# Optimization experiments

Hardware: AMD Instinct MI355X
Metric: run time of the kernel (lower is better)

Reference implementation:

```python
import jax, jax.numpy as jnp
import numpy as np

N_NODES = 50000
EPS_BN = 1e-5


def _glorot(key, shape):
    fan_in, fan_out = shape[0], shape[1]
    lim = jnp.sqrt(6.0 / (fan_in + fan_out))
    return jax.random.uniform(key, shape, jnp.float32, -lim, lim)


def setup_inputs() -> dict:
    key = jax.random.key(0)
    ks = jax.random.split(key, 12)
    x = jax.random.normal(ks[0], (N_NODES, 128), jnp.float32)
    y = jax.random.normal(ks[1], (256, 1), jnp.float32)
    edge_index = jax.random.randint(ks[2], (2, 800000), 0, N_NODES, jnp.int64)
    return {
        "x": x,
        "y": y,
        "edge_index": edge_index,
        # GCNConv weights (in_dim, out_dim) + bias
        "W1": _glorot(ks[3], (128, 128)), "b1": jnp.zeros((128,), jnp.float32),
        "W2": _glorot(ks[4], (128, 128)), "b2": jnp.zeros((128,), jnp.float32),
        "W3": _glorot(ks[5], (128, 64)),  "b3": jnp.zeros((64,), jnp.float32),
        # target MLP: BatchNorm1d(1) -> Linear(1,128) -> ReLU -> Dropout -> Linear(128,64)
        "bn_gamma": jnp.ones((1,), jnp.float32), "bn_beta": jnp.zeros((1,), jnp.float32),
        "Wm1": _glorot(ks[6], (1, 128)),  "bm1": jnp.zeros((128,), jnp.float32),
        "Wm2": _glorot(ks[7], (128, 64)), "bm2": jnp.zeros((64,), jnp.float32),
    }


def gcn_conv(h, W, b, src, dst, deg_isqrt, n):
    # PyG GCNConv: x' = D^-1/2 (A+I) D^-1/2 (x W) + b, self-loops included in src/dst
    h = h @ W  # [n, out]
    norm = (deg_isqrt[src] * deg_isqrt[dst])[:, None]  # [E, 1]
    msg = h[src] * norm  # gather + scale, [E, out]
    out = jax.ops.segment_sum(msg, dst, num_segments=n)  # scatter-add
    return out + b


def reference(x, y, edge_index, W1, b1, W2, b2, W3, b3, bn_gamma, bn_beta, Wm1, bm1, Wm2, bm2):
    n = x.shape[0]
    loops = jnp.arange(n, dtype=edge_index.dtype)
    src = jnp.concatenate([edge_index[0], loops])
    dst = jnp.concatenate([edge_index[1], loops])
    deg = jax.ops.segment_sum(jnp.ones_like(dst, dtype=x.dtype), dst, num_segments=n)
    deg_isqrt = jnp.where(deg > 0, jax.lax.rsqrt(deg), 0.0)

    h = jax.nn.relu(gcn_conv(x, W1, b1, src, dst, deg_isqrt, n))
    h = jax.nn.relu(gcn_conv(h, W2, b2, src, dst, deg_isqrt, n))
    h = gcn_conv(h, W3, b3, src, dst, deg_isqrt, n)
    # transform_feat: normalize per-node embeddings (global_mean_pool result is discarded in source)
    x_emb = h / jnp.clip(jnp.linalg.norm(h, axis=1, keepdims=True), 1e-12)

    # target branch: BatchNorm1d (training-mode batch stats), Linear, ReLU, Dropout(eval=id), Linear
    mu = jnp.mean(y, axis=0, keepdims=True)
    var = jnp.var(y, axis=0, keepdims=True)
    yb = (y - mu) * jax.lax.rsqrt(var + EPS_BN) * bn_gamma + bn_beta
    t = jax.nn.relu(yb @ Wm1 + bm1)
    t = t @ Wm2 + bm2
    y_emb = t / jnp.clip(jnp.linalg.norm(t, axis=1, keepdims=True), 1e-12)
    return (x_emb, y_emb)
```

## Files before the change

kernel.cpp:

```cpp
#include <hip/hip_runtime.h>
#include <hip/hip_bf16.h>

typedef __attribute__((ext_vector_type(8))) short short8;
typedef __attribute__((ext_vector_type(4))) float f32x4;

__device__ __forceinline__ ushort f2bf(float f) {
    union { float f; uint u; } v; v.f = f;
    uint u = v.u;
    return (ushort)((u + 0x7fffu + ((u >> 16) & 1u)) >> 16);
}
__device__ __forceinline__ float bf_lo(uint u) { return __uint_as_float(u << 16); }
__device__ __forceinline__ float bf_hi(uint u) { return __uint_as_float(u & 0xffff0000u); }
__device__ __forceinline__ float lane_bcast_f(float v, int j) {
    return __uint_as_float(__builtin_amdgcn_readlane(__float_as_uint(v), j));
}

template <int COLS, bool F32IN>
__device__ __forceinline__ void gemm_body(const void* __restrict__ Xin,
                                          const ushort* __restrict__ Wt,
                                          ushort* __restrict__ Y, int n,
                                          int bid, char* smem) {
    constexpr int LDW = 136;
    ushort* sX = (ushort*)smem;
    ushort* sW = sX + 64 * LDW;
    const int tid = threadIdx.x;
    const int row0 = bid * 64;

    if (F32IN) {
        const float* Xf = (const float*)Xin;
#pragma unroll
        for (int i = 0; i < 8; ++i) {
            int idx = i * 256 + tid;
            int r = idx >> 5, kc = idx & 31;
            int gr = min(row0 + r, n - 1);
            float4 v = *(const float4*)&Xf[(size_t)gr * 128 + kc * 4];
            ushort4 o;
            o.x = f2bf(v.x); o.y = f2bf(v.y); o.z = f2bf(v.z); o.w = f2bf(v.w);
            *(ushort4*)&sX[r * LDW + kc * 4] = o;
        }
    } else {
        const ushort* Xb = (const ushort*)Xin;
#pragma unroll
        for (int i = 0; i < 4; ++i) {
            int idx = i * 256 + tid;
            int r = idx >> 4, kc = idx & 15;
            int gr = min(row0 + r, n - 1);
            uint4 v = *(const uint4*)&Xb[(size_t)gr * 128 + kc * 8];
            *(uint4*)&sX[r * LDW + kc * 8] = v;
        }
    }
#pragma unroll
    for (int c = tid; c < COLS * 16; c += 256) {
        int r = c >> 4, kc = c & 15;
        uint4 v = *(const uint4*)&Wt[(size_t)r * 128 + kc * 8];
        *(uint4*)&sW[r * LDW + kc * 8] = v;
    }
    __syncthreads();

    constexpr int NT = (COLS == 128) ? 2 : 1;
    constexpr int WN = COLS / 4;
    const int w = tid >> 6;
    const int lane = tid & 63;
    const int lm = lane & 15;
    const int kq = lane >> 4;

    f32x4 acc[4][NT];
#pragma unroll
    for (int mt = 0; mt < 4; ++mt)
#pragma unroll
        for (int ntn = 0; ntn < NT; ++ntn) acc[mt][ntn] = (f32x4){0.f, 0.f, 0.f, 0.f};

#pragma unroll
    for (int ks = 0; ks < 4; ++ks) {
        const int k0 = ks * 32 + kq * 8;
        short8 bfr[NT];
#pragma unroll
        for (int ntn = 0; ntn < NT; ++ntn)
            bfr[ntn] = *(const short8*)&sW[(w * WN + ntn * 16 + lm) * LDW + k0];
#pragma unroll
        for (int mt = 0; mt < 4; ++mt) {
            short8 afr = *(const short8*)&sX[(mt * 16 + lm) * LDW + k0];
#pragma unroll
            for (int ntn = 0; ntn < NT; ++ntn)
                acc[mt][ntn] = __builtin_amdgcn_mfma_f32_16x16x32_bf16(afr, bfr[ntn], acc[mt][ntn], 0, 0, 0);
        }
    }

#pragma unroll
    for (int mt = 0; mt < 4; ++mt) {
        int r_base = row0 + mt * 16 + kq * 4;
#pragma unroll
        for (int ntn = 0; ntn < NT; ++ntn) {
            int col = w * WN + ntn * 16 + lm;
#pragma unroll
            for (int rr = 0; rr < 4; ++rr) {
                int r = r_base + rr;
                if (r < n) Y[(size_t)r * COLS + col] = f2bf(acc[mt][ntn][rr]);
            }
        }
    }
}

#define PCHUNK 4096

__global__ __launch_bounds__(256) void k_partition(const int* __restrict__ src,
                                                   const int* __restrict__ dst, int E,
                                                   int nbuck, int cap, int pblocks,
                                                   int* __restrict__ gcur,
                                                   uint* __restrict__ part,
                                                   const float* __restrict__ W1,
                                                   const float* __restrict__ W2,
                                                   const float* __restrict__ W3,
                                                   ushort* __restrict__ wt1,
                                                   ushort* __restrict__ wt2,
                                                   ushort* __restrict__ wt3) {
    __shared__ int hist[256];
    __shared__ int base[256];
    __shared__ int cnt2[256];
    const int tid = threadIdx.x;

    if ((int)blockIdx.x >= pblocks) {
        int i = (blockIdx.x - pblocks) * 256 + tid;
        if (i < 16384) {
            int k = i >> 7, nn = i & 127;
            wt1[nn * 128 + k] = f2bf(W1[i]);
        } else if (i < 32768) {
            int j = i - 16384;
            int k = j >> 7, nn = j & 127;
            wt2[nn * 128 + k] = f2bf(W2[j]);
        } else if (i < 40960) {
            int j = i - 32768;
            int k = j >> 6, nn = j & 63;
            wt3[nn * 128 + k] = f2bf(W3[j]);
        }
        return;
    }

    const int s0 = blockIdx.x * PCHUNK;
    const int send = min(s0 + PCHUNK, E);
    hist[tid] = 0;
    cnt2[tid] = 0;
    __syncthreads();
    for (int i = s0 + tid; i < send; i += 256) {
        int d = dst[i];
        atomicAdd(&hist[d >> 8], 1);
    }
    __syncthreads();
    if (tid < nbuck && hist[tid] > 0) base[tid] = atomicAdd(&gcur[tid], hist[tid]);
    __syncthreads();
    for (int i = s0 + tid; i < send; i += 256) {
        int d = dst[i];
        int s = src[i];
        int k = d >> 8;
        int r = base[k] + atomicAdd(&cnt2[k], 1);
        if (r < cap) part[(size_t)k * cap + r] = ((uint)d << 16) | (uint)s;
    }
}

__global__ __launch_bounds__(256) void k_sort_gemm1(const uint* __restrict__ part,
                                                    const int* __restrict__ gcur,
                                                    int nbuck, int cap, int n,
                                                    int* __restrict__ rowptr,
                                                    float* __restrict__ dis,
                                                    int* __restrict__ csr,
                                                    const float* __restrict__ x,
                                                    const ushort* __restrict__ wt1,
                                                    ushort* __restrict__ bufA) {
    __shared__ char smem[(64 + 128) * 136 * 2];
    const int tid = threadIdx.x;

    if ((int)blockIdx.x >= nbuck) {
        gemm_body<128, true>(x, wt1, bufA, n, blockIdx.x - nbuck, smem);
        return;
    }

    int* hist  = (int*)smem;
    int* pfx   = hist + 256;
    int* sscan = pfx + 256;
    const int b = blockIdx.x;

    int gv = (tid < nbuck) ? min(gcur[tid], cap) : 0;
    sscan[tid] = gv;
    __syncthreads();
    for (int off = 1; off < 256; off <<= 1) {
        int t = (tid >= off) ? sscan[tid - off] : 0;
        __syncthreads();
        sscan[tid] += t;
        __syncthreads();
    }
    const int outbase = (b == 0) ? 0 : sscan[b - 1];
    const int sz = min(gcur[b], cap);
    const uint* seg = part + (size_t)b * cap;

    hist[tid] = 0;
    __syncthreads();
    for (int i = tid; i < sz; i += 256) atomicAdd(&hist[(seg[i] >> 16) & 255], 1);
    __syncthreads();

    int cnt_t = hist[tid];
    pfx[tid] = cnt_t;
    __syncthreads();
    for (int off = 1; off < 256; off <<= 1) {
        int t = (tid >= off) ? pfx[tid - off] : 0;
        __syncthreads();
        pfx[tid] += t;
        __syncthreads();
    }
    int excl = pfx[tid] - cnt_t;

    int node = b * 256 + tid;
    if (node < n) {
        rowptr[node] = outbase + excl;
        dis[node] = rsqrtf((float)(cnt_t + 1));
        if (node == n - 1) rowptr[n] = outbase + excl + cnt_t;
    }
    __syncthreads();
    pfx[tid] = excl;
    hist[tid] = 0;
    __syncthreads();
    for (int i = tid; i < sz; i += 256) {
        uint p = seg[i];
        int j = (p >> 16) & 255;
        int r = atomicAdd(&hist[j], 1);
        csr[outbase + pfx[j] + r] = (int)(p & 0xffffu);
    }
}

template <int COLS>
__global__ __launch_bounds__(512) void agg_gemm(const ushort* __restrict__ H,
                                                const float* __restrict__ dis,
                                                const int* __restrict__ rowptr,
                                                const int* __restrict__ csr,
                                                const float* __restrict__ bias,
                                                const ushort* __restrict__ Wt,
                                                ushort* __restrict__ Y, int n) {
    __shared__ ushort sX[64 * 136];
    const int tid = threadIdx.x;
    const int wv = tid >> 6;
    const int lane = tid & 63;
    const int row0 = blockIdx.x * 64;
    const uint* Hu = (const uint*)H;
    const float2 bv = ((const float2*)bias)[lane];

#pragma unroll 1
    for (int i = 0; i < 8; ++i) {
        const int lr = wv * 8 + i;
        const int v = min(row0 + lr, n - 1);
        const float dv = dis[v];
        const int e0 = rowptr[v];
        const int e1 = rowptr[v + 1];
        uint h0 = Hu[(size_t)v * 64 + lane];
        float ax = dv * bf_lo(h0), ay = dv * bf_hi(h0);

        int e = e0;
        while (e < e1) {
            const int c = min(e1 - e, 64);
            int sidx = 0; float sw = 0.0f;
            if (lane < c) { sidx = csr[e + lane]; sw = dis[sidx]; }
            int j = 0;
            for (; j + 16 <= c; j += 16) {
                uint hv[16]; float wgt[16];
#pragma unroll
                for (int u = 0; u < 16; ++u) {
                    int s = __builtin_amdgcn_readlane(sidx, j + u);
                    wgt[u] = lane_bcast_f(sw, j + u);
                    hv[u] = Hu[(size_t)s * 64 + lane];
                }
#pragma unroll
                for (int u = 0; u < 16; ++u) { ax += wgt[u] * bf_lo(hv[u]); ay += wgt[u] * bf_hi(hv[u]); }
            }
            for (; j + 4 <= c; j += 4) {
                uint hv[4]; float wgt[4];
#pragma unroll
                for (int u = 0; u < 4; ++u) {
                    int s = __builtin_amdgcn_readlane(sidx, j + u);
                    wgt[u] = lane_bcast_f(sw, j + u);
                    hv[u] = Hu[(size_t)s * 64 + lane];
                }
#pragma unroll
                for (int u = 0; u < 4; ++u) { ax += wgt[u] * bf_lo(hv[u]); ay += wgt[u] * bf_hi(hv[u]); }
            }
            for (; j < c; ++j) {
                int s = __builtin_amdgcn_readlane(sidx, j);
                float wg = lane_bcast_f(sw, j);
                uint hh = Hu[(size_t)s * 64 + lane];
                ax += wg * bf_lo(hh); ay += wg * bf_hi(hh);
            }
            e += c;
        }

        float rx = fmaxf(dv * ax + bv.x, 0.f);
        float ry = fmaxf(dv * ay + bv.y, 0.f);
        ((uint*)sX)[lr * 68 + lane] = (uint)f2bf(rx) | ((uint)f2bf(ry) << 16);
    }
    __syncthreads();

    constexpr int NT = COLS / 64;
    constexpr int WN = COLS / 4;
    const int wr = wv >> 2;
    const int wc = wv & 3;
    const int lm = lane & 15;
    const int kq = lane >> 4;

    f32x4 acc[2][NT];
#pragma unroll
    for (int mt = 0; mt < 2; ++mt)
#pragma unroll
        for (int ntn = 0; ntn < NT; ++ntn) acc[mt][ntn] = (f32x4){0.f, 0.f, 0.f, 0.f};

#pragma unroll
    for (int ks = 0; ks < 4; ++ks) {
        const int k0 = ks * 32 + kq * 8;
        short8 bfr[NT];
#pragma unroll
        for (int ntn = 0; ntn < NT; ++ntn)
            bfr[ntn] = *(const short8*)&Wt[(size_t)(wc * WN + ntn * 16 + lm) * 128 + k0];
#pragma unroll
        for (int mt = 0; mt < 2; ++mt) {
            short8 afr = *(const short8*)&sX[((wr * 2 + mt) * 16 + lm) * 136 + k0];
#pragma unroll
            for (int ntn = 0; ntn < NT; ++ntn)
                acc[mt][ntn] = __builtin_amdgcn_mfma_f32_16x16x32_bf16(afr, bfr[ntn], acc[mt][ntn], 0, 0, 0);
        }
    }

#pragma unroll
    for (int mt = 0; mt < 2; ++mt) {
        int r_base = row0 + (wr * 2 + mt) * 16 + kq * 4;
#pragma unroll
        for (int ntn = 0; ntn < NT; ++ntn) {
            int col = wc * WN + ntn * 16 + lm;
#pragma unroll
            for (int rr = 0; rr < 4; ++rr) {
                int r = r_base + rr;
                if (r < n) Y[(size_t)r * COLS + col] = f2bf(acc[mt][ntn][rr]);
            }
        }
    }
}

__global__ __launch_bounds__(256) void agg64_final(const ushort* __restrict__ H,
                                                   const float* __restrict__ dis,
                                                   const int* __restrict__ rowptr,
                                                   const int* __restrict__ csr,
                                                   const float* __restrict__ bias,
                                                   float* __restrict__ out, int n, int agrid,
                                                   const float* __restrict__ y,
                                                   const float* __restrict__ gamma,
                                                   const float* __restrict__ beta,
                                                   const float* __restrict__ Wm1,
                                                   const float* __restrict__ bm1,
                                                   const float* __restrict__ Wm2,
                                                   const float* __restrict__ bm2,
                                                   float* __restrict__ out_y) {
    __shared__ float red[256];
    __shared__ float t1[128];
    __shared__ float s_mu, s_var;
    const int tid = threadIdx.x;

    if ((int)blockIdx.x >= agrid) {
        float yv = y[tid];
        red[tid] = yv;
        __syncthreads();
        for (int s = 128; s > 0; s >>= 1) {
            if (tid < s) red[tid] += red[tid + s];
            __syncthreads();
        }
        if (tid == 0) s_mu = red[0] * (1.0f / 256.0f);
        __syncthreads();
        float mu = s_mu;
        float d = yv - mu;
        red[tid] = d * d;
        __syncthreads();
        for (int s = 128; s > 0; s >>= 1) {
            if (tid < s) red[tid] += red[tid + s];
            __syncthreads();
        }
        if (tid == 0) s_var = red[0] * (1.0f / 256.0f);
        __syncthreads();

        const int row = blockIdx.x - agrid;
        float yb = (y[row] - mu) * rsqrtf(s_var + 1e-5f) * gamma[0] + beta[0];
        if (tid < 128) t1[tid] = fmaxf(yb * Wm1[tid] + bm1[tid], 0.0f);
        __syncthreads();
        if (tid < 64) {
            float acc = bm2[tid];
#pragma unroll 8
            for (int c = 0; c < 128; ++c) acc += t1[c] * Wm2[c * 64 + tid];
            float ss = acc * acc;
#pragma unroll
            for (int m = 1; m < 64; m <<= 1) ss += __shfl_xor(ss, m, 64);
            out_y[row * 64 + tid] = acc / fmaxf(sqrtf(ss), 1e-12f);
        }
        return;
    }

    const int wid = blockIdx.x * 4 + (tid >> 6);
    const int lane = tid & 63;
    if (wid >= n) return;
    const int v = wid;
    const float dv = dis[v];
    const int e0 = rowptr[v];
    const int e1 = rowptr[v + 1];

    float acc = dv * bf_lo((uint)H[(size_t)v * 64 + lane]);

    int e = e0;
    while (e < e1) {
        const int c = min(e1 - e, 64);
        int sidx = 0; float sw = 0.0f;
        if (lane < c) { sidx = csr[e + lane]; sw = dis[sidx]; }
        int j = 0;
        for (; j + 16 <= c; j += 16) {
            ushort hv[16]; float w[16];
#pragma unroll
            for (int u = 0; u < 16; ++u) {
                int s = __builtin_amdgcn_readlane(sidx, j + u);
                w[u] = lane_bcast_f(sw, j + u);
                hv[u] = H[(size_t)s * 64 + lane];
            }
#pragma unroll
            for (int u = 0; u < 16; ++u) acc += w[u] * bf_lo((uint)hv[u]);
        }
        for (; j < c; ++j) {
            int s = __builtin_amdgcn_readlane(sidx, j);
            float w = lane_bcast_f(sw, j);
            acc += w * bf_lo((uint)H[(size_t)s * 64 + lane]);
        }
        e += c;
    }

    float r = dv * acc + bias[lane];
    float ss = r * r;
#pragma unroll
    for (int m = 1; m < 64; m <<= 1) ss += __shfl_xor(ss, m, 64);
    r = r / fmaxf(sqrtf(ss), 1e-12f);
    out[(size_t)v * 64 + lane] = r;
}

extern "C" void kernel_launch(void* const* d_in, const int* in_sizes, int n_in,
                              void* d_out, int out_size, void* d_ws, size_t ws_size,
                              hipStream_t stream) {
    const float* x     = (const float*)d_in[0];
    const float* y     = (const float*)d_in[1];
    const int*   edge  = (const int*)d_in[2];
    const float* W1    = (const float*)d_in[3];
    const float* b1    = (const float*)d_in[4];
    const float* W2    = (const float*)d_in[5];
    const float* b2    = (const float*)d_in[6];
    const float* W3    = (const float*)d_in[7];
    const float* b3    = (const float*)d_in[8];
    const float* bng   = (const float*)d_in[9];
    const float* bnb   = (const float*)d_in[10];
    const float* Wm1   = (const float*)d_in[11];
    const float* bm1   = (const float*)d_in[12];
    const float* Wm2   = (const float*)d_in[13];
    const float* bm2   = (const float*)d_in[14];

    const int n = in_sizes[0] / 128;
    const int E = in_sizes[2] / 2;
    const int* src = edge;
    const int* dst = edge + E;

    const int nbuck = (n + 255) / 256;
    const int cap = E / nbuck + E / nbuck / 4 + 1024;

    size_t off = 0;
    auto carve = [&](size_t bytes) {
        size_t p = off;
        off = (off + bytes + 255) & ~(size_t)255;
        return p;
    };
    char* ws = (char*)d_ws;
    int*    gcur    = (int*)(ws + carve(256 * 4));
    uint*   part    = (uint*)(ws + carve((size_t)nbuck * cap * 4));
    int*    rowptr  = (int*)(ws + carve((size_t)(n + 1) * 4));
    int*    csr     = (int*)(ws + carve((size_t)E * 4));
    float*  dis     = (float*)(ws + carve((size_t)n * 4));
    ushort* wt1     = (ushort*)(ws + carve(128 * 128 * 2));
    ushort* wt2     = (ushort*)(ws + carve(128 * 128 * 2));
    ushort* wt3     = (ushort*)(ws + carve(64 * 128 * 2));
    ushort* bufA    = (ushort*)(ws + carve((size_t)n * 128 * 2));
    ushort* bufB    = (ushort*)(ws + carve((size_t)n * 128 * 2));
    ushort* bufC    = (ushort*)(ws + carve((size_t)n * 64 * 2));
    (void)ws_size; (void)n_in; (void)out_size;

    float* x_emb = (float*)d_out;
    float* y_emb = (float*)d_out + (size_t)n * 64;

    const int pblocks = (E + PCHUNK - 1) / PCHUNK;
    const int ggrid = (n + 63) / 64;
    const int agrid = (n + 3) / 4;

    hipMemsetAsync(gcur, 0, 256 * 4, stream);
    k_partition<<<pblocks + 160, 256, 0, stream>>>(src, dst, E, nbuck, cap, pblocks,
                                                   gcur, part, W1, W2, W3, wt1, wt2, wt3);
    k_sort_gemm1<<<nbuck + ggrid, 256, 0, stream>>>(part, gcur, nbuck, cap, n,
                                                    rowptr, dis, csr, x, wt1, bufA);

    agg_gemm<128><<<ggrid, 512, 0, stream>>>(bufA, dis, rowptr, csr, b1, wt2, bufB, n);
    agg_gemm<64><<<ggrid, 512, 0, stream>>>(bufB, dis, rowptr, csr, b2, wt3, bufC, n);
    agg64_final<<<agrid + 256, 256, 0, stream>>>(bufC, dis, rowptr, csr, b3, x_emb, n, agrid,
                                                 y, bng, bnb, Wm1, bm1, Wm2, bm2, y_emb);
}
```

Baseline: 245.4 us.

## Fold source-degree scaling into GEMM epilogue and prefetch next row's edge list

The agg_gemm epilogue now multiplies each output row by its own dis, so the next layer's features come pre-scaled by the source normalization. The layer-2 aggregation and the final aggregation therefore skip the per-edge dis gather and the per-edge weight multiply. agg_gemm also loads rowptr and dis for its 8 rows in one shot and software-prefetches the next row's CSR chunk while the current row is processed. PCHUNK shrinks to 1024 to spread partitioning over more blocks. This removes random dis reads per edge, at the cost of extra registers and rounding differences from scaling before the bf16 conversion.

```diff
diff --git a/kernel.cpp b/kernel.cpp
--- a/kernel.cpp
+++ b/kernel.cpp
@@ -101,7 +101,7 @@
     }
 }
 
-#define PCHUNK 4096
+#define PCHUNK 1024
 
 __global__ __launch_bounds__(256) void k_partition(const int* __restrict__ src,
                                                    const int* __restrict__ dst, int E,
@@ -226,7 +226,7 @@
     }
 }
 
-template <int COLS>
+template <int COLS, bool WITHDIS>
 __global__ __launch_bounds__(512) void agg_gemm(const ushort* __restrict__ H,
                                                 const float* __restrict__ dis,
                                                 const int* __restrict__ rowptr,
@@ -242,56 +242,92 @@
     const uint* Hu = (const uint*)H;
     const float2 bv = ((const float2*)bias)[lane];
 
+    const int vb = row0 + wv * 8;
+    int rpv = 0;
+    if (lane < 9) rpv = rowptr[min(vb + lane, n)];
+    float dvv = (lane < 8) ? dis[min(vb + lane, n - 1)] : 0.0f;
+
+    int nx_e0 = __builtin_amdgcn_readlane(rpv, 0);
+    int nx_e1 = __builtin_amdgcn_readlane(rpv, 1);
+    int nx_c  = min(nx_e1 - nx_e0, 64);
+    int nx_s = 0; float nx_w = 0.0f;
+    if (lane < nx_c) {
+        nx_s = csr[nx_e0 + lane];
+        if (WITHDIS) nx_w = dis[nx_s];
+    }
+
 #pragma unroll 1
     for (int i = 0; i < 8; ++i) {
-        const int lr = wv * 8 + i;
-        const int v = min(row0 + lr, n - 1);
-        const float dv = dis[v];
-        const int e0 = rowptr[v];
-        const int e1 = rowptr[v + 1];
+        const int v = min(vb + i, n - 1);
         uint h0 = Hu[(size_t)v * 64 + lane];
-        float ax = dv * bf_lo(h0), ay = dv * bf_hi(h0);
-
-        int e = e0;
-        while (e < e1) {
-            const int c = min(e1 - e, 64);
-            int sidx = 0; float sw = 0.0f;
-            if (lane < c) { sidx = csr[e + lane]; sw = dis[sidx]; }
+        const float dv = lane_bcast_f(dvv, i);
+        int e1 = nx_e1, c = nx_c;
+        int e = nx_e0;
+        int sidx = nx_s; float sw = nx_w;
+        if (i < 7) {
+            nx_e0 = __builtin_amdgcn_readlane(rpv, i + 1);
+            nx_e1 = __builtin_amdgcn_readlane(rpv, i + 2);
+            nx_c = min(nx_e1 - nx_e0, 64);
+            nx_s = 0; nx_w = 0.0f;
+            if (lane < nx_c) {
+                nx_s = csr[nx_e0 + lane];
+                if (WITHDIS) nx_w = dis[nx_s];
+            }
+        }
+
+        float ax = 0.f, ay = 0.f;
+        for (;;) {
             int j = 0;
             for (; j + 16 <= c; j += 16) {
                 uint hv[16]; float wgt[16];
 #pragma unroll
                 for (int u = 0; u < 16; ++u) {
                     int s = __builtin_amdgcn_readlane(sidx, j + u);
-                    wgt[u] = lane_bcast_f(sw, j + u);
+                    if (WITHDIS) wgt[u] = lane_bcast_f(sw, j + u);
                     hv[u] = Hu[(size_t)s * 64 + lane];
                 }
 #pragma unroll
-                for (int u = 0; u < 16; ++u) { ax += wgt[u] * bf_lo(hv[u]); ay += wgt[u] * bf_hi(hv[u]); }
+                for (int u = 0; u < 16; ++u) {
+                    if (WITHDIS) { ax += wgt[u] * bf_lo(hv[u]); ay += wgt[u] * bf_hi(hv[u]); }
+                    else         { ax += bf_lo(hv[u]);          ay += bf_hi(hv[u]); }
+                }
             }
             for (; j + 4 <= c; j += 4) {
                 uint hv[4]; float wgt[4];
 #pragma unroll
                 for (int u = 0; u < 4; ++u) {
                     int s = __builtin_amdgcn_readlane(sidx, j + u);
-                    wgt[u] = lane_bcast_f(sw, j + u);
+                    if (WITHDIS) wgt[u] = lane_bcast_f(sw, j + u);
                     hv[u] = Hu[(size_t)s * 64 + lane];
                 }
 #pragma unroll
-                for (int u = 0; u < 4; ++u) { ax += wgt[u] * bf_lo(hv[u]); ay += wgt[u] * bf_hi(hv[u]); }
+                for (int u = 0; u < 4; ++u) {
+                    if (WITHDIS) { ax += wgt[u] * bf_lo(hv[u]); ay += wgt[u] * bf_hi(hv[u]); }
+                    else         { ax += bf_lo(hv[u]);          ay += bf_hi(hv[u]); }
+                }
             }
             for (; j < c; ++j) {
                 int s = __builtin_amdgcn_readlane(sidx, j);
-                float wg = lane_bcast_f(sw, j);
                 uint hh = Hu[(size_t)s * 64 + lane];
-                ax += wg * bf_lo(hh); ay += wg * bf_hi(hh);
+                if (WITHDIS) {
+                    float wg = lane_bcast_f(sw, j);
+                    ax += wg * bf_lo(hh); ay += wg * bf_hi(hh);
+                } else {
+                    ax += bf_lo(hh); ay += bf_hi(hh);
+                }
             }
             e += c;
-        }
-
+            if (e >= e1) break;
+            c = min(e1 - e, 64);
+            sidx = 0; sw = 0.0f;
+            if (lane < c) { sidx = csr[e + lane]; if (WITHDIS) sw = dis[sidx]; }
+        }
+
+        if (WITHDIS) { ax += dv * bf_lo(h0); ay += dv * bf_hi(h0); }
+        else         { ax += bf_lo(h0);      ay += bf_hi(h0); }
         float rx = fmaxf(dv * ax + bv.x, 0.f);
         float ry = fmaxf(dv * ay + bv.y, 0.f);
-        ((uint*)sX)[lr * 68 + lane] = (uint)f2bf(rx) | ((uint)f2bf(ry) << 16);
+        ((uint*)sX)[(wv * 8 + i) * 68 + lane] = (uint)f2bf(rx) | ((uint)f2bf(ry) << 16);
     }
     __syncthreads();
 
@@ -328,12 +364,15 @@
     for (int mt = 0; mt < 2; ++mt) {
         int r_base = row0 + (wr * 2 + mt) * 16 + kq * 4;
 #pragma unroll
-        for (int ntn = 0; ntn < NT; ++ntn) {
-            int col = wc * WN + ntn * 16 + lm;
-#pragma unroll
-            for (int rr = 0; rr < 4; ++rr) {
-                int r = r_base + rr;
-                if (r < n) Y[(size_t)r * COLS + col] = f2bf(acc[mt][ntn][rr]);
+        for (int rr = 0; rr < 4; ++rr) {
+            int r = r_base + rr;
+            if (r < n) {
+                float dr = dis[r];
+#pragma unroll
+                for (int ntn = 0; ntn < NT; ++ntn) {
+                    int col = wc * WN + ntn * 16 + lm;
+                    Y[(size_t)r * COLS + col] = f2bf(acc[mt][ntn][rr] * dr);
+                }
             }
         }
     }
@@ -400,36 +439,35 @@
     if (wid >= n) return;
     const int v = wid;
     const float dv = dis[v];
+    uint h0 = (uint)H[(size_t)v * 64 + lane];
     const int e0 = rowptr[v];
     const int e1 = rowptr[v + 1];
 
-    float acc = dv * bf_lo((uint)H[(size_t)v * 64 + lane]);
-
+    float acc = 0.0f;
     int e = e0;
     while (e < e1) {
         const int c = min(e1 - e, 64);
-        int sidx = 0; float sw = 0.0f;
-        if (lane < c) { sidx = csr[e + lane]; sw = dis[sidx]; }
+        int sidx = 0;
+        if (lane < c) sidx = csr[e + lane];
         int j = 0;
         for (; j + 16 <= c; j += 16) {
-            ushort hv[16]; float w[16];
+            ushort hv[16];
 #pragma unroll
             for (int u = 0; u < 16; ++u) {
                 int s = __builtin_amdgcn_readlane(sidx, j + u);
-                w[u] = lane_bcast_f(sw, j + u);
                 hv[u] = H[(size_t)s * 64 + lane];
             }
 #pragma unroll
-            for (int u = 0; u < 16; ++u) acc += w[u] * bf_lo((uint)hv[u]);
+            for (int u = 0; u < 16; ++u) acc += bf_lo((uint)hv[u]);
         }
         for (; j < c; ++j) {
             int s = __builtin_amdgcn_readlane(sidx, j);
-            float w = lane_bcast_f(sw, j);
-            acc += w * bf_lo((uint)H[(size_t)s * 64 + lane]);
+            acc += bf_lo((uint)H[(size_t)s * 64 + lane]);
         }
         e += c;
     }
 
+    acc += bf_lo(h0);
     float r = dv * acc + bias[lane];
     float ss = r * r;
 #pragma unroll
@@ -498,8 +536,8 @@
     k_sort_gemm1<<<nbuck + ggrid, 256, 0, stream>>>(part, gcur, nbuck, cap, n,
                                                     rowptr, dis, csr, x, wt1, bufA);
 
-    agg_gemm<128><<<ggrid, 512, 0, stream>>>(bufA, dis, rowptr, csr, b1, wt2, bufB, n);
-    agg_gemm<64><<<ggrid, 512, 0, stream>>>(bufB, dis, rowptr, csr, b2, wt3, bufC, n);
+    agg_gemm<128, true><<<ggrid, 512, 0, stream>>>(bufA, dis, rowptr, csr, b1, wt2, bufB, n);
+    agg_gemm<64, false><<<ggrid, 512, 0, stream>>>(bufB, dis, rowptr, csr, b2, wt3, bufC, n);
     agg64_final<<<agrid + 256, 256, 0, stream>>>(bufC, dis, rowptr, csr, b3, x_emb, n, agrid,
                                                  y, bng, bnb, Wm1, bm1, Wm2, bm2, y_emb);
 }
```

Measured after the change: 259.7 us. +5.9%, slower.

## Fold source-side degree normalization into GEMM epilogue and drop per-edge weight gathers

Applied to the files above, without the earlier changes.

Source-node normalization D^-1/2 is now applied once per row in the GEMM output epilogue, so aggregation becomes a plain unweighted sum of gathered rows and no longer loads dis[src] per edge or broadcasts weights with readlane. Degrees are counted with global atomics in the partition kernel, so the first GEMM can scale its output without waiting for the sort kernel, and PCHUNK is reduced for more partition blocks. Tail edges are handled by a masked 16-wide gather instead of 4-wide and scalar loops. In exchange it adds global atomic traffic on deg, a larger memset, and wasted loads in the masked tail.

```diff
diff --git a/kernel.cpp b/kernel.cpp
--- a/kernel.cpp
+++ b/kernel.cpp
@@ -11,15 +11,13 @@
 }
 __device__ __forceinline__ float bf_lo(uint u) { return __uint_as_float(u << 16); }
 __device__ __forceinline__ float bf_hi(uint u) { return __uint_as_float(u & 0xffff0000u); }
-__device__ __forceinline__ float lane_bcast_f(float v, int j) {
-    return __uint_as_float(__builtin_amdgcn_readlane(__float_as_uint(v), j));
-}
 
 template <int COLS, bool F32IN>
 __device__ __forceinline__ void gemm_body(const void* __restrict__ Xin,
                                           const ushort* __restrict__ Wt,
                                           ushort* __restrict__ Y, int n,
-                                          int bid, char* smem) {
+                                          int bid, char* smem,
+                                          const int* __restrict__ deg) {
     constexpr int LDW = 136;
     ushort* sX = (ushort*)smem;
     ushort* sW = sX + 64 * LDW;
@@ -90,24 +88,28 @@
     for (int mt = 0; mt < 4; ++mt) {
         int r_base = row0 + mt * 16 + kq * 4;
 #pragma unroll
-        for (int ntn = 0; ntn < NT; ++ntn) {
-            int col = w * WN + ntn * 16 + lm;
-#pragma unroll
-            for (int rr = 0; rr < 4; ++rr) {
-                int r = r_base + rr;
-                if (r < n) Y[(size_t)r * COLS + col] = f2bf(acc[mt][ntn][rr]);
-            }
-        }
-    }
-}
-
-#define PCHUNK 4096
+        for (int rr = 0; rr < 4; ++rr) {
+            int r = r_base + rr;
+            if (r < n) {
+                float dr = rsqrtf((float)(deg[r] + 1));
+#pragma unroll
+                for (int ntn = 0; ntn < NT; ++ntn) {
+                    int col = w * WN + ntn * 16 + lm;
+                    Y[(size_t)r * COLS + col] = f2bf(acc[mt][ntn][rr] * dr);
+                }
+            }
+        }
+    }
+}
+
+#define PCHUNK 1024
 
 __global__ __launch_bounds__(256) void k_partition(const int* __restrict__ src,
                                                    const int* __restrict__ dst, int E,
                                                    int nbuck, int cap, int pblocks,
                                                    int* __restrict__ gcur,
                                                    uint* __restrict__ part,
+                                                   int* __restrict__ deg,
                                                    const float* __restrict__ W1,
                                                    const float* __restrict__ W2,
                                                    const float* __restrict__ W3,
@@ -144,6 +146,7 @@
     for (int i = s0 + tid; i < send; i += 256) {
         int d = dst[i];
         atomicAdd(&hist[d >> 8], 1);
+        atomicAdd(&deg[d], 1);
     }
     __syncthreads();
     if (tid < nbuck && hist[tid] > 0) base[tid] = atomicAdd(&gcur[tid], hist[tid]);
@@ -161,16 +164,16 @@
                                                     const int* __restrict__ gcur,
                                                     int nbuck, int cap, int n,
                                                     int* __restrict__ rowptr,
-                                                    float* __restrict__ dis,
                                                     int* __restrict__ csr,
                                                     const float* __restrict__ x,
                                                     const ushort* __restrict__ wt1,
-                                                    ushort* __restrict__ bufA) {
+                                                    ushort* __restrict__ bufA,
+                                                    const int* __restrict__ deg) {
     __shared__ char smem[(64 + 128) * 136 * 2];
     const int tid = threadIdx.x;
 
     if ((int)blockIdx.x >= nbuck) {
-        gemm_body<128, true>(x, wt1, bufA, n, blockIdx.x - nbuck, smem);
+        gemm_body<128, true>(x, wt1, bufA, n, blockIdx.x - nbuck, smem, deg);
         return;
     }
 
@@ -211,7 +214,6 @@
     int node = b * 256 + tid;
     if (node < n) {
         rowptr[node] = outbase + excl;
-        dis[node] = rsqrtf((float)(cnt_t + 1));
         if (node == n - 1) rowptr[n] = outbase + excl + cnt_t;
     }
     __syncthreads();
@@ -228,7 +230,7 @@
 
 template <int COLS>
 __global__ __launch_bounds__(512) void agg_gemm(const ushort* __restrict__ H,
-                                                const float* __restrict__ dis,
+                                                const int* __restrict__ deg,
                                                 const int* __restrict__ rowptr,
                                                 const int* __restrict__ csr,
                                                 const float* __restrict__ bias,
@@ -241,57 +243,54 @@
     const int row0 = blockIdx.x * 64;
     const uint* Hu = (const uint*)H;
     const float2 bv = ((const float2*)bias)[lane];
+    const int vb = row0 + wv * 8;
 
 #pragma unroll 1
     for (int i = 0; i < 8; ++i) {
-        const int lr = wv * 8 + i;
-        const int v = min(row0 + lr, n - 1);
-        const float dv = dis[v];
+        const int v = min(vb + i, n - 1);
+        uint h0 = Hu[(size_t)v * 64 + lane];
+        const int dgv = deg[v];
         const int e0 = rowptr[v];
         const int e1 = rowptr[v + 1];
-        uint h0 = Hu[(size_t)v * 64 + lane];
-        float ax = dv * bf_lo(h0), ay = dv * bf_hi(h0);
-
+
+        float ax = 0.f, ay = 0.f;
         int e = e0;
         while (e < e1) {
             const int c = min(e1 - e, 64);
-            int sidx = 0; float sw = 0.0f;
-            if (lane < c) { sidx = csr[e + lane]; sw = dis[sidx]; }
+            int sidx = 0;
+            if (lane < c) sidx = csr[e + lane];
             int j = 0;
             for (; j + 16 <= c; j += 16) {
-                uint hv[16]; float wgt[16];
+                uint hv[16];
 #pragma unroll
                 for (int u = 0; u < 16; ++u) {
                     int s = __builtin_amdgcn_readlane(sidx, j + u);
-                    wgt[u] = lane_bcast_f(sw, j + u);
                     hv[u] = Hu[(size_t)s * 64 + lane];
                 }
 #pragma unroll
-                for (int u = 0; u < 16; ++u) { ax += wgt[u] * bf_lo(hv[u]); ay += wgt[u] * bf_hi(hv[u]); }
-            }
-            for (; j + 4 <= c; j += 4) {
-                uint hv[4]; float wgt[4];
-#pragma unroll
-                for (int u = 0; u < 4; ++u) {
+                for (int u = 0; u < 16; ++u) { ax += bf_lo(hv[u]); ay += bf_hi(hv[u]); }
+            }
+            if (j < c) {
+                uint hv[16];
+#pragma unroll
+                for (int u = 0; u < 16; ++u) {
                     int s = __builtin_amdgcn_readlane(sidx, j + u);
-                    wgt[u] = lane_bcast_f(sw, j + u);
                     hv[u] = Hu[(size_t)s * 64 + lane];
                 }
 #pragma unroll
-                for (int u = 0; u < 4; ++u) { ax += wgt[u] * bf_lo(hv[u]); ay += wgt[u] * bf_hi(hv[u]); }
-            }
-            for (; j < c; ++j) {
-                int s = __builtin_amdgcn_readlane(sidx, j);
-                float wg = lane_bcast_f(sw, j);
-                uint hh = Hu[(size_t)s * 64 + lane];
-                ax += wg * bf_lo(hh); ay += wg * bf_hi(hh);
+                for (int u = 0; u < 16; ++u) {
+                    uint hm = (j + u < c) ? hv[u] : 0u;
+                    ax += bf_lo(hm); ay += bf_hi(hm);
+                }
             }
             e += c;
         }
 
+        ax += bf_lo(h0); ay += bf_hi(h0);
+        const float dv = rsqrtf((float)(dgv + 1));
         float rx = fmaxf(dv * ax + bv.x, 0.f);
         float ry = fmaxf(dv * ay + bv.y, 0.f);
-        ((uint*)sX)[lr * 68 + lane] = (uint)f2bf(rx) | ((uint)f2bf(ry) << 16);
+        ((uint*)sX)[(wv * 8 + i) * 68 + lane] = (uint)f2bf(rx) | ((uint)f2bf(ry) << 16);
     }
     __syncthreads();
 
@@ -328,19 +327,22 @@
     for (int mt = 0; mt < 2; ++mt) {
         int r_base = row0 + (wr * 2 + mt) * 16 + kq * 4;
 #pragma unroll
-        for (int ntn = 0; ntn < NT; ++ntn) {
-            int col = wc * WN + ntn * 16 + lm;
-#pragma unroll
-            for (int rr = 0; rr < 4; ++rr) {
-                int r = r_base + rr;
-                if (r < n) Y[(size_t)r * COLS + col] = f2bf(acc[mt][ntn][rr]);
+        for (int rr = 0; rr < 4; ++rr) {
+            int r = r_base + rr;
+            if (r < n) {
+                float dr = rsqrtf((float)(deg[r] + 1));
+#pragma unroll
+                for (int ntn = 0; ntn < NT; ++ntn) {
+                    int col = wc * WN + ntn * 16 + lm;
+                    Y[(size_t)r * COLS + col] = f2bf(acc[mt][ntn][rr] * dr);
+                }
             }
         }
     }
 }
 
 __global__ __launch_bounds__(256) void agg64_final(const ushort* __restrict__ H,
-                                                   const float* __restrict__ dis,
+                                                   const int* __restrict__ deg,
                                                    const int* __restrict__ rowptr,
                                                    const int* __restrict__ csr,
                                                    const float* __restrict__ bias,
@@ -399,37 +401,46 @@
     const int lane = tid & 63;
     if (wid >= n) return;
     const int v = wid;
-    const float dv = dis[v];
+    ushort h0 = H[(size_t)v * 64 + lane];
+    const int dgv = deg[v];
     const int e0 = rowptr[v];
     const int e1 = rowptr[v + 1];
 
-    float acc = dv * bf_lo((uint)H[(size_t)v * 64 + lane]);
-
+    float acc = 0.0f;
     int e = e0;
     while (e < e1) {
         const int c = min(e1 - e, 64);
-        int sidx = 0; float sw = 0.0f;
-        if (lane < c) { sidx = csr[e + lane]; sw = dis[sidx]; }
+        int sidx = 0;
+        if (lane < c) sidx = csr[e + lane];
         int j = 0;
         for (; j + 16 <= c; j += 16) {
-            ushort hv[16]; float w[16];
+            ushort hv[16];
 #pragma unroll
             for (int u = 0; u < 16; ++u) {
                 int s = __builtin_amdgcn_readlane(sidx, j + u);
-                w[u] = lane_bcast_f(sw, j + u);
                 hv[u] = H[(size_t)s * 64 + lane];
             }
 #pragma unroll
-            for (int u = 0; u < 16; ++u) acc += w[u] * bf_lo((uint)hv[u]);
-        }
-        for (; j < c; ++j) {
-            int s = __builtin_amdgcn_readlane(sidx, j);
-            float w = lane_bcast_f(sw, j);
-            acc += w * bf_lo((uint)H[(size_t)s * 64 + lane]);
+            for (int u = 0; u < 16; ++u) acc += bf_lo((uint)hv[u]);
+        }
+        if (j < c) {
+            ushort hv[16];
+#pragma unroll
+            for (int u = 0; u < 16; ++u) {
+                int s = __builtin_amdgcn_readlane(sidx, j + u);
+                hv[u] = H[(size_t)s * 64 + lane];
+            }
+#pragma unroll
+            for (int u = 0; u < 16; ++u) {
+                uint hm = (j + u < c) ? (uint)hv[u] : 0u;
+                acc += bf_lo(hm);
+            }
         }
         e += c;
     }
 
+    acc += bf_lo((uint)h0);
+    const float dv = rsqrtf((float)(dgv + 1));
     float r = dv * acc + bias[lane];
     float ss = r * r;
 #pragma unroll
@@ -473,10 +484,10 @@
     };
     char* ws = (char*)d_ws;
     int*    gcur    = (int*)(ws + carve(256 * 4));
+    int*    deg     = (int*)(ws + carve((size_t)n * 4));
     uint*   part    = (uint*)(ws + carve((size_t)nbuck * cap * 4));
     int*    rowptr  = (int*)(ws + carve((size_t)(n + 1) * 4));
     int*    csr     = (int*)(ws + carve((size_t)E * 4));
-    float*  dis     = (float*)(ws + carve((size_t)n * 4));
     ushort* wt1     = (ushort*)(ws + carve(128 * 128 * 2));
     ushort* wt2     = (ushort*)(ws + carve(128 * 128 * 2));
     ushort* wt3     = (ushort*)(ws + carve(64 * 128 * 2));
@@ -492,14 +503,14 @@
     const int ggrid = (n + 63) / 64;
     const int agrid = (n + 3) / 4;
 
-    hipMemsetAsync(gcur, 0, 256 * 4, stream);
+    hipMemsetAsync(gcur, 0, 1024 + (size_t)n * 4, stream);
     k_partition<<<pblocks + 160, 256, 0, stream>>>(src, dst, E, nbuck, cap, pblocks,
-                                                   gcur, part, W1, W2, W3, wt1, wt2, wt3);
+                                                   gcur, part, deg, W1, W2, W3, wt1, wt2, wt3);
     k_sort_gemm1<<<nbuck + ggrid, 256, 0, stream>>>(part, gcur, nbuck, cap, n,
-                                                    rowptr, dis, csr, x, wt1, bufA);
-
-    agg_gemm<128><<<ggrid, 512, 0, stream>>>(bufA, dis, rowptr, csr, b1, wt2, bufB, n);
-    agg_gemm<64><<<ggrid, 512, 0, stream>>>(bufB, dis, rowptr, csr, b2, wt3, bufC, n);
-    agg64_final<<<agrid + 256, 256, 0, stream>>>(bufC, dis, rowptr, csr, b3, x_emb, n, agrid,
+                                                    rowptr, csr, x, wt1, bufA, deg);
+
+    agg_gemm<128><<<ggrid, 512, 0, stream>>>(bufA, deg, rowptr, csr, b1, wt2, bufB, n);
+    agg_gemm<64><<<ggrid, 512, 0, stream>>>(bufB, deg, rowptr, csr, b2, wt3, bufC, n);
+    agg64_final<<<agrid + 256, 256, 0, stream>>>(bufC, deg, rowptr, csr, b3, x_emb, n, agrid,
                                                  y, bng, bnb, Wm1, bm1, Wm2, bm2, y_emb);
 }
```

Result: slower. 295.4 us (+20.4%).

## Fold source-degree normalization into GEMM epilogue to skip per-edge dis gathers

Applied to the files above, without the earlier changes.

Each GEMM epilogue now multiplies its output rows by dis[r]. The layer-2 and layer-3 aggregations can then sum neighbour features without gathering dis[src] per edge. The remainder loops are merged into one masked 16-wide loop; tail slots load row 0 and are zeroed by the mask or by a zero weight. The partition chunk size also drops from 4096 to 1024 for more partition blocks. The trade-off is some wasted tail loads and a little epilogue work in exchange for removing a random gather per edge.

```diff
diff --git a/kernel.cpp b/kernel.cpp
--- a/kernel.cpp
+++ b/kernel.cpp
@@ -101,7 +101,7 @@
     }
 }
 
-#define PCHUNK 4096
+#define PCHUNK 1024
 
 __global__ __launch_bounds__(256) void k_partition(const int* __restrict__ src,
                                                    const int* __restrict__ dst, int E,
@@ -226,7 +226,7 @@
     }
 }
 
-template <int COLS>
+template <int COLS, bool WITHDIS>
 __global__ __launch_bounds__(512) void agg_gemm(const ushort* __restrict__ H,
                                                 const float* __restrict__ dis,
                                                 const int* __restrict__ rowptr,
@@ -241,57 +241,49 @@
     const int row0 = blockIdx.x * 64;
     const uint* Hu = (const uint*)H;
     const float2 bv = ((const float2*)bias)[lane];
+    const int vb = row0 + wv * 8;
 
 #pragma unroll 1
     for (int i = 0; i < 8; ++i) {
-        const int lr = wv * 8 + i;
-        const int v = min(row0 + lr, n - 1);
+        const int v = min(vb + i, n - 1);
+        uint h0 = Hu[(size_t)v * 64 + lane];
         const float dv = dis[v];
         const int e0 = rowptr[v];
         const int e1 = rowptr[v + 1];
-        uint h0 = Hu[(size_t)v * 64 + lane];
-        float ax = dv * bf_lo(h0), ay = dv * bf_hi(h0);
-
+
+        float ax = 0.f, ay = 0.f;
         int e = e0;
         while (e < e1) {
             const int c = min(e1 - e, 64);
             int sidx = 0; float sw = 0.0f;
-            if (lane < c) { sidx = csr[e + lane]; sw = dis[sidx]; }
-            int j = 0;
-            for (; j + 16 <= c; j += 16) {
+            if (lane < c) { sidx = csr[e + lane]; if (WITHDIS) sw = dis[sidx]; }
+#pragma unroll 1
+            for (int j = 0; j < c; j += 16) {
                 uint hv[16]; float wgt[16];
 #pragma unroll
                 for (int u = 0; u < 16; ++u) {
                     int s = __builtin_amdgcn_readlane(sidx, j + u);
-                    wgt[u] = lane_bcast_f(sw, j + u);
+                    if (WITHDIS) wgt[u] = lane_bcast_f(sw, j + u);
                     hv[u] = Hu[(size_t)s * 64 + lane];
                 }
 #pragma unroll
-                for (int u = 0; u < 16; ++u) { ax += wgt[u] * bf_lo(hv[u]); ay += wgt[u] * bf_hi(hv[u]); }
-            }
-            for (; j + 4 <= c; j += 4) {
-                uint hv[4]; float wgt[4];
-#pragma unroll
-                for (int u = 0; u < 4; ++u) {
-                    int s = __builtin_amdgcn_readlane(sidx, j + u);
-                    wgt[u] = lane_bcast_f(sw, j + u);
-                    hv[u] = Hu[(size_t)s * 64 + lane];
+                for (int u = 0; u < 16; ++u) {
+                    if (WITHDIS) {
+                        ax += wgt[u] * bf_lo(hv[u]); ay += wgt[u] * bf_hi(hv[u]);
+                    } else {
+                        uint hm = (j + u < c) ? hv[u] : 0u;
+                        ax += bf_lo(hm); ay += bf_hi(hm);
+                    }
                 }
-#pragma unroll
-                for (int u = 0; u < 4; ++u) { ax += wgt[u] * bf_lo(hv[u]); ay += wgt[u] * bf_hi(hv[u]); }
-            }
-            for (; j < c; ++j) {
-                int s = __builtin_amdgcn_readlane(sidx, j);
-                float wg = lane_bcast_f(sw, j);
-                uint hh = Hu[(size_t)s * 64 + lane];
-                ax += wg * bf_lo(hh); ay += wg * bf_hi(hh);
             }
             e += c;
         }
 
+        if (WITHDIS) { ax += dv * bf_lo(h0); ay += dv * bf_hi(h0); }
+        else         { ax += bf_lo(h0);      ay += bf_hi(h0); }
         float rx = fmaxf(dv * ax + bv.x, 0.f);
         float ry = fmaxf(dv * ay + bv.y, 0.f);
-        ((uint*)sX)[lr * 68 + lane] = (uint)f2bf(rx) | ((uint)f2bf(ry) << 16);
+        ((uint*)sX)[(wv * 8 + i) * 68 + lane] = (uint)f2bf(rx) | ((uint)f2bf(ry) << 16);
     }
     __syncthreads();
 
@@ -328,12 +320,15 @@
     for (int mt = 0; mt < 2; ++mt) {
         int r_base = row0 + (wr * 2 + mt) * 16 + kq * 4;
 #pragma unroll
-        for (int ntn = 0; ntn < NT; ++ntn) {
-            int col = wc * WN + ntn * 16 + lm;
-#pragma unroll
-            for (int rr = 0; rr < 4; ++rr) {
-                int r = r_base + rr;
-                if (r < n) Y[(size_t)r * COLS + col] = f2bf(acc[mt][ntn][rr]);
+        for (int rr = 0; rr < 4; ++rr) {
+            int r = r_base + rr;
+            if (r < n) {
+                float dr = dis[r];
+#pragma unroll
+                for (int ntn = 0; ntn < NT; ++ntn) {
+                    int col = wc * WN + ntn * 16 + lm;
+                    Y[(size_t)r * COLS + col] = f2bf(acc[mt][ntn][rr] * dr);
+                }
             }
         }
     }
@@ -399,37 +394,35 @@
     const int lane = tid & 63;
     if (wid >= n) return;
     const int v = wid;
+    ushort h0 = H[(size_t)v * 64 + lane];
     const float dv = dis[v];
     const int e0 = rowptr[v];
     const int e1 = rowptr[v + 1];
 
-    float acc = dv * bf_lo((uint)H[(size_t)v * 64 + lane]);
-
+    float acc = 0.0f;
     int e = e0;
     while (e < e1) {
         const int c = min(e1 - e, 64);
-        int sidx = 0; float sw = 0.0f;
-        if (lane < c) { sidx = csr[e + lane]; sw = dis[sidx]; }
-        int j = 0;
-        for (; j + 16 <= c; j += 16) {
-            ushort hv[16]; float w[16];
+        int sidx = 0;
+        if (lane < c) sidx = csr[e + lane];
+#pragma unroll 1
+        for (int j = 0; j < c; j += 16) {
+            ushort hv[16];
 #pragma unroll
             for (int u = 0; u < 16; ++u) {
                 int s = __builtin_amdgcn_readlane(sidx, j + u);
-                w[u] = lane_bcast_f(sw, j + u);
                 hv[u] = H[(size_t)s * 64 + lane];
             }
 #pragma unroll
-            for (int u = 0; u < 16; ++u) acc += w[u] * bf_lo((uint)hv[u]);
-        }
-        for (; j < c; ++j) {
-            int s = __builtin_amdgcn_readlane(sidx, j);
-            float w = lane_bcast_f(sw, j);
-            acc += w * bf_lo((uint)H[(size_t)s * 64 + lane]);
+            for (int u = 0; u < 16; ++u) {
+                uint hm = (j + u < c) ? (uint)hv[u] : 0u;
+                acc += bf_lo(hm);
+            }
         }
         e += c;
     }
 
+    acc += bf_lo((uint)h0);
     float r = dv * acc + bias[lane];
     float ss = r * r;
 #pragma unroll
@@ -498,8 +491,8 @@
     k_sort_gemm1<<<nbuck + ggrid, 256, 0, stream>>>(part, gcur, nbuck, cap, n,
                                                     rowptr, dis, csr, x, wt1, bufA);
 
-    agg_gemm<128><<<ggrid, 512, 0, stream>>>(bufA, dis, rowptr, csr, b1, wt2, bufB, n);
-    agg_gemm<64><<<ggrid, 512, 0, stream>>>(bufB, dis, rowptr, csr, b2, wt3, bufC, n);
+    agg_gemm<128, true><<<ggrid, 512, 0, stream>>>(bufA, dis, rowptr, csr, b1, wt2, bufB, n);
+    agg_gemm<64, false><<<ggrid, 512, 0, stream>>>(bufB, dis, rowptr, csr, b2, wt3, bufC, n);
     agg64_final<<<agrid + 256, 256, 0, stream>>>(bufC, dis, rowptr, csr, b3, x_emb, n, agrid,
                                                  y, bng, bnb, Wm1, bm1, Wm2, bm2, y_emb);
 }
```

Result: slower. 253.0 us (+3.1%).
